# Optimization experiments

Hardware: AMD Instinct MI355X
Metric: run time of the kernel (lower is better)

The kernel has to match this reference:

```python
import jax, jax.numpy as jnp
import numpy as np

N_WG = 512      # waveguides n
N_COL = 512     # mesh columns
M = N_WG // 2   # node slots per column (odd columns have one masked dummy)
N_NODE = N_COL * M
B = 8192        # batch of input fields
PI4 = np.pi / 4


def build_mesh_indices():
    """Rectangular (Clements-style) mesh: per-column (top, bottom, mask) arrays."""
    top = np.zeros((N_COL, M), np.int32)
    bottom = np.zeros((N_COL, M), np.int32)
    mask = np.zeros((N_COL, M), np.int32)
    for c in range(N_COL):
        if c % 2 == 0:
            t = np.arange(0, N_WG, 2, dtype=np.int32)
            top[c], bottom[c], mask[c] = t, t + 1, 1
        else:
            t = np.arange(1, N_WG - 1, 2, dtype=np.int32)
            k = len(t)
            top[c, :k], bottom[c, :k], mask[c, :k] = t, t + 1, 1
            # masked dummy slot uses otherwise-unused rows 0 and N_WG-1
            top[c, k:], bottom[c, k:] = 0, N_WG - 1
    return jnp.asarray(top), jnp.asarray(bottom), jnp.asarray(mask)


def setup_inputs() -> dict:
    key = jax.random.key(0)
    ks = jax.random.split(key, 6)
    top, bottom, mask = build_mesh_indices()
    return {
        "x": jax.random.normal(ks[0], (N_WG, B), dtype=jnp.float32),
        "thetas": 2 * np.pi * jax.random.uniform(ks[1], (N_NODE,), dtype=jnp.float32),
        "phis": 2 * np.pi * jax.random.uniform(ks[2], (N_NODE,), dtype=jnp.float32),
        "gammas": 2 * np.pi * jax.random.uniform(ks[3], (N_WG,), dtype=jnp.float32),
        "bs_errors": 0.01 * jax.random.normal(ks[4], (N_NODE, 2), dtype=jnp.float32),
        "loss_errors": -0.1 * jax.random.uniform(ks[5], (N_NODE, 2), dtype=jnp.float32),
        "top": top, "bottom": bottom, "mask": mask,
    }


def _dc_terms(bs_errors, loss_errors, side):
    """_parallel_dc: per-node directional-coupler 2x2 elements [N,4] complex."""
    ins = jnp.exp(jnp.log(10.0) * loss_errors[:, side] / 20.0)
    e = bs_errors[:, side]
    s, c = jnp.sin(PI4 + e), jnp.cos(PI4 + e)
    t11 = (ins * s).astype(jnp.complex64)
    t12 = ins * (1j * c)
    t21 = (1j * c).astype(jnp.complex64)
    t22 = s.astype(jnp.complex64)
    return jnp.stack([t11, t12, t21, t22], axis=-1)


def _transform(v, T, t, b, m):
    """_parallel_transform: masked 2x2 gather-multiply-scatter. T: [M,4] complex."""
    vt, vb = v[t], v[b]
    one_m = 1.0 - m
    s11 = (T[:, 0] * m + one_m)[:, None]
    s12 = (T[:, 1] * m)[:, None]
    s21 = (T[:, 2] * m)[:, None]
    s22 = (T[:, 3] * m + one_m)[:, None]
    return v.at[t].set(s11 * vt + s21 * vb).at[b].set(s12 * vt + s22 * vb)


def reference(x, thetas, phis, gammas, bs_errors, loss_errors, top, bottom, mask):
    # input gamma phase screen, then propagate through all mesh columns
    v = x.astype(jnp.complex64) * jnp.exp(1j * gammas)[:, None]          # [n, B]
    left = _dc_terms(bs_errors, loss_errors, 0).reshape(N_COL, M, 4)
    right = _dc_terms(bs_errors, loss_errors, 1).reshape(N_COL, M, 4)
    th = thetas.reshape(N_COL, M)
    ph = phis.reshape(N_COL, M)
    mf = mask.astype(jnp.float32)

    def column(v, xs):
        t, b, m, thc, phc, L, R = xs
        # PhaseStyle.TOP, forward: phi -> left DC -> theta -> right DC
        v = v.at[t].multiply(jnp.exp(1j * phc * m)[:, None])
        v = _transform(v, L, t, b, m)
        v = v.at[t].multiply(jnp.exp(1j * thc * m)[:, None])
        v = _transform(v, R, t, b, m)
        return v, None

    v, _ = jax.lax.scan(column, v, (top, bottom, mf, th, ph, left, right))
    return jnp.stack([v.real, v.imag])  # [2, n, B]
```

## Files before the change

kernel.cpp:

```cpp
#include <hip/hip_runtime.h>
#include <math.h>

#define BATCH 8192
#define NROW 512
#define NCOL 512
#define MNODE 256

typedef __attribute__((ext_vector_type(8))) short bf16x8;
typedef __attribute__((ext_vector_type(4))) float f32x4;

__device__ __forceinline__ short2 split1(float x) {
  unsigned u = __float_as_uint(x);
  short h = (short)(u >> 16);
  float r = x - __uint_as_float(u & 0xffff0000u);
  short l = (short)(__float_as_uint(r) >> 16);
  return make_short2(h, l);
}

__global__ __launch_bounds__(256) void precomp_kernel(
    const float* __restrict__ thetas, const float* __restrict__ phis,
    const float* __restrict__ bse, const float* __restrict__ lse,
    float4* __restrict__ pp) {
  int n = blockIdx.x * 256 + threadIdx.x;
  float th = thetas[n], ph = phis[n];
  float e0 = bse[2 * n + 0], e1 = bse[2 * n + 1];
  float l0 = lse[2 * n + 0], l1 = lse[2 * n + 1];
  const float K = 0.16609640474436813f;
  float ins0 = exp2f(l0 * K), ins1 = exp2f(l1 * K);
  const float PI4 = 0.7853981633974483f;
  float s0, c0, s1, c1, sp, cp, st, ct;
  sincosf(PI4 + e0, &s0, &c0);
  sincosf(PI4 + e1, &s1, &c1);
  sincosf(ph, &sp, &cp);
  sincosf(th, &st, &ct);
  float AL = ins0 * s0, C1L = c0, C2L = ins0 * c0, SL = s0;
  float AR = ins1 * s1, C1R = c1, C2R = ins1 * c1, SR = s1;
  float a11r = AL * cp,   a11i = AL * sp;
  float a12r = 0.f,       a12i = C1L;
  float a21r = -C2L * sp, a21i = C2L * cp;
  float a22r = SL,        a22i = 0.f;
  float b11r = a11r * ct - a11i * st, b11i = a11r * st + a11i * ct;
  float b12r = a12r * ct - a12i * st, b12i = a12r * st + a12i * ct;
  float n11r = AR * b11r - C1R * a21i;
  float n11i = AR * b11i + C1R * a21r;
  float n12r = AR * b12r - C1R * a22i;
  float n12i = AR * b12i + C1R * a22r;
  float n21r = -C2R * b11i + SR * a21r;
  float n21i =  C2R * b11r + SR * a21i;
  float n22r = -C2R * b12i + SR * a22r;
  float n22i =  C2R * b12r + SR * a22i;
  pp[2 * n + 0] = make_float4(n11r, n11i, n12r, n12i);
  pp[2 * n + 1] = make_float4(n21r, n21i, n22r, n22i);
}

__device__ __forceinline__ void proc_pair(float& vtr, float& vti, float& vbr, float& vbi,
                                          const float4 q0, const float4 q1) {
  float tr = q0.x * vtr - q0.y * vti + q0.z * vbr - q0.w * vbi;
  float ti = q0.x * vti + q0.y * vtr + q0.z * vbi + q0.w * vbr;
  float br = q1.x * vtr - q1.y * vti + q1.z * vbr - q1.w * vbi;
  float bi = q1.x * vti + q1.y * vtr + q1.z * vbi + q1.w * vbr;
  vtr = tr; vti = ti; vbr = br; vbi = bi;
}

__device__ __forceinline__ int swz(int b) { return b ^ ((b >> 3) & 7); }

__global__ __launch_bounds__(256) void compose_band(
    const float* __restrict__ gammas, const float4* __restrict__ pp,
    float* __restrict__ Tsegs, int P) {
  __shared__ float ep[5120];

  const int tid  = threadIdx.x;
  const int lane = tid & 63;
  const int w    = tid >> 6;
  const int seg  = blockIdx.x >> 7;
  const int g    = blockIdx.x & 127;
  const int col  = g * 4 + w;

  const float4* ps = pp + (size_t)seg * P * 1024;
  float* T = Tsegs + (size_t)seg * (1024 * NROW);

  const int colA = (col - 63) & ~1;
  const int E    = colA + 2 * lane;
  const int je   = E >> 1;
  const int jeC  = je < 0 ? 0 : (je > 255 ? 255 : je);

  const bool vE  = (E >= 0) && (E <= 510);
  const bool vOT = (E >= 0) && (E <= 508);
  const bool vOB = (E >= 2) && (E <= 510);

  float ar = 0.f, ai = 0.f, br = 0.f, bi = 0.f;
  {
    float vr0 = 1.f, vi0 = 0.f;
    if (seg == 0) {
      float sg, cg;
      sincosf(gammas[col], &sg, &cg);
      vr0 = cg; vi0 = sg;
    }
    if (E == col)     { ar = vr0; ai = vi0; }
    if (E + 1 == col) { br = vr0; bi = vi0; }
  }

  const float4* pe = ps + 2 * jeC;
  const float4* po = ps + 512 + 2 * jeC;

  float sar = 0.f, sai = 0.f, sbr = 0.f, sbi = 0.f;

  for (int p = 0; p < P; ++p) {
    float4 q0 = pe[0];
    float4 q1 = pe[1];
    float4 o0 = po[0];
    float4 o1 = po[-1];
    pe += 1024; po += 1024;

    {
      float tr = q0.x * ar - q0.y * ai + q0.z * br - q0.w * bi;
      float ti = q0.x * ai + q0.y * ar + q0.z * bi + q0.w * br;
      float ur = q1.x * ar - q1.y * ai + q1.z * br - q1.w * bi;
      float ui = q1.x * ai + q1.y * ar + q1.z * bi + q1.w * br;
      if (vE) { ar = tr; ai = ti; br = ur; bi = ui; }
    }

    if (p == P - 1) { sar = ar; sai = ai; sbr = br; sbi = bi; }

    float anr = __shfl_down(ar, 1, 64);
    float ani = __shfl_down(ai, 1, 64);
    float bpr = __shfl_up(br, 1, 64);
    float bpi = __shfl_up(bi, 1, 64);
    if (lane == 63) { anr = 0.f; ani = 0.f; }
    if (lane == 0)  { bpr = 0.f; bpi = 0.f; }
    {
      float tr = o0.x * br - o0.y * bi + o0.z * anr - o0.w * ani;
      float ti = o0.x * bi + o0.y * br + o0.z * ani + o0.w * anr;
      float ur = o1.x * bpr - o1.y * bpi + o1.z * ar - o1.w * ai;
      float ui = o1.x * bpi + o1.y * bpr + o1.z * ai + o1.w * ar;
      if (vOT) { br = tr; bi = ti; }
      if (vOB) { ar = ur; ai = ui; }
    }
  }

  int sprow = -1;
  float spr = 0.f, spi = 0.f;
  if ((col & 1) == 0) {
    if (colA + 128 <= 511) {
      sprow = colA + 128;
      float4 w1 = ps[(size_t)(P - 1) * 1024 + 512 + 2 * (colA / 2 + 63) + 1];
      float vtr = __shfl(sbr, 63, 64);
      float vti = __shfl(sbi, 63, 64);
      spr = w1.x * vtr - w1.y * vti;
      spi = w1.x * vti + w1.y * vtr;
    }
  } else {
    if (colA - 1 >= 0) {
      sprow = colA - 1;
      float4 w0 = ps[(size_t)(P - 1) * 1024 + 512 + 2 * (colA / 2 - 1)];
      float vbr = __shfl(sar, 0, 64);
      float vbi = __shfl(sai, 0, 64);
      spr = w0.z * vbr - w0.w * vbi;
      spi = w0.z * vbi + w0.w * vbr;
    }
  }

  for (int i = tid; i < 5120; i += 256) ep[i] = 0.f;
  __syncthreads();
  if (E >= 0 && E <= 510) {
    ep[E * 5 + w]         = ar;
    ep[(512 + E) * 5 + w] = ai;
    ep[(E + 1) * 5 + w]       = br;
    ep[(513 + E) * 5 + w]     = bi;
  }
  if (lane == 0 && sprow >= 0) {
    ep[sprow * 5 + w]         = spr;
    ep[(512 + sprow) * 5 + w] = spi;
  }
  __syncthreads();
#pragma unroll
  for (int k = 0; k < 4; ++k) {
    const int i = k * 256 + tid;
    *(float4*)(T + (size_t)i * NROW + g * 4) =
        make_float4(ep[i * 5 + 0], ep[i * 5 + 1], ep[i * 5 + 2], ep[i * 5 + 3]);
  }
}

__global__ __launch_bounds__(256) void compose_kernel(
    const float* __restrict__ gammas, const float4* __restrict__ pp,
    float* __restrict__ Tsegs, int pairs_per_seg) {
  __shared__ float4 buf[2][1024];
  float* epf = (float*)buf;

  const int tid  = threadIdx.x;
  const int lane = tid & 63;
  const int w    = tid >> 6;
  const int seg  = blockIdx.x >> 7;
  const int g    = blockIdx.x & 127;
  const int col  = g * 4 + w;
  const int colmin = g * 4;

  const float4* ps = pp + (size_t)seg * pairs_per_seg * 1024;
  float* T = Tsegs + (size_t)seg * (1024 * NROW);

  float vr[8], vi[8];
#pragma unroll
  for (int r = 0; r < 8; ++r) {
    const int row = lane * 8 + r;
    vr[r] = 0.f; vi[r] = 0.f;
    if (row == col) {
      if (seg == 0) {
        float sg, cg;
        sincosf(gammas[row], &sg, &cg);
        vr[r] = cg; vi[r] = sg;
      } else {
        vr[r] = 1.f;
      }
    }
  }

  {
    const int sw = swz(tid);
#pragma unroll
    for (int k = 0; k < 4; ++k)
      buf[0][256 * k + sw] = ps[256 * k + tid];
  }
  __syncthreads();

  const int Lc = col >> 3;

#pragma unroll 1
  for (int p = 0; p < pairs_per_seg; ++p) {
    const int b = p & 1;

    const int HA = (p >> 2) + 3;
    const bool act  = (lane >= Lc - HA)     && (lane <= Lc + HA);
    const bool wide = (lane >= Lc - HA - 1) && (lane <= Lc + HA + 1);

    float4 f0, f1, f2, f3;
    bool st0 = false, st1 = false;
    if (p < pairs_per_seg - 1) {
      const int slo = colmin - 2 * p - 50;
      const int shi = colmin + 2 * p + 53;
      st0 = (tid + 1 >= slo) && (tid <= shi);
      st1 = (tid + 257 >= slo) && (tid + 256 <= shi);
      const float4* src = ps + (size_t)(p + 1) * 1024;
      if (st0) { f0 = src[tid];       f2 = src[512 + tid]; }
      if (st1) { f1 = src[256 + tid]; f3 = src[768 + tid]; }
    }

    float4 pe[8], po[7], pu1;
    if (act) {
      const int base = 8 * lane;
      const int l7 = lane & 7;
#pragma unroll
      for (int j = 0; j < 8; ++j) pe[j] = buf[b][base + (j ^ l7)];
#pragma unroll
      for (int j = 0; j < 7; ++j) po[j] = buf[b][512 + base + (j ^ l7)];
      const int lm = (lane == 0) ? 0 : lane - 1;
      pu1 = buf[b][512 + 8 * lm + (7 ^ (lm & 7))];

#pragma unroll
      for (int k = 0; k < 4; ++k)
        proc_pair(vr[2 * k], vi[2 * k], vr[2 * k + 1], vi[2 * k + 1],
                  pe[2 * k], pe[2 * k + 1]);

#pragma unroll
      for (int k = 0; k < 3; ++k)
        proc_pair(vr[2 * k + 1], vi[2 * k + 1], vr[2 * k + 2], vi[2 * k + 2],
                  po[2 * k], po[2 * k + 1]);
    }

    float br = 0.f, bi = 0.f, tu = 0.f, tv = 0.f;
    if (wide) {
      br = __shfl_down(vr[0], 1, 64);
      bi = __shfl_down(vi[0], 1, 64);
      tu = __shfl_up(vr[7], 1, 64);
      tv = __shfl_up(vi[7], 1, 64);
    }
    if (act) {
      float nAr = po[6].x * vr[7] - po[6].y * vi[7] + po[6].z * br - po[6].w * bi;
      float nAi = po[6].x * vi[7] + po[6].y * vr[7] + po[6].z * bi + po[6].w * br;
      float nBr = pu1.x * tu - pu1.y * tv + pu1.z * vr[0] - pu1.w * vi[0];
      float nBi = pu1.x * tv + pu1.y * tu + pu1.z * vi[0] + pu1.w * vr[0];
      if (lane < 63) { vr[7] = nAr; vi[7] = nAi; }
      if (lane > 0)  { vr[0] = nBr; vi[0] = nBi; }
    }

    if (p < pairs_per_seg - 1) {
      const int sw = swz(tid);
      if (st0) { buf[1 - b][sw] = f0;       buf[1 - b][512 + sw] = f2; }
      if (st1) { buf[1 - b][256 + sw] = f1; buf[1 - b][768 + sw] = f3; }
    }
    __syncthreads();
  }

#pragma unroll
  for (int r = 0; r < 8; ++r) {
    epf[(lane * 8 + r) * 5 + w] = vr[r];
    epf[(512 + lane * 8 + r) * 5 + w] = vi[r];
  }
  __syncthreads();
#pragma unroll
  for (int k = 0; k < 4; ++k) {
    const int i = k * 256 + tid;
    *(float4*)(T + (size_t)i * NROW + g * 4) =
        make_float4(epf[i * 5 + 0], epf[i * 5 + 1], epf[i * 5 + 2], epf[i * 5 + 3]);
  }
}

__global__ __launch_bounds__(256) void merge_g(
    const float* __restrict__ Ab, const float* __restrict__ Bb,
    float* __restrict__ Cb, long sA, long sB, long sC, int HA, int HB) {
  const float* A = Ab + (long)blockIdx.z * sA;
  const float* B = Bb + (long)blockIdx.z * sB;
  float*       C = Cb + (long)blockIdx.z * sC;

  __shared__ short sAh[64 * 40], sAl[64 * 40];

  const int tid = threadIdx.x;
  const int lane = tid & 63;
  const int w = tid >> 6;
  const int bm = blockIdx.y * 64;
  const int bn = blockIdx.x * 64;
  const int wm = (w & 1) * 32;
  const int wn = (w >> 1) * 32;
  const int q = lane >> 4;
  const int l15 = lane & 15;

  const int sm = tid >> 2;
  const int sk = (tid & 3) * 8;

  const int rmin = (blockIdx.y & 7) * 64;
  int klo = rmin - HA;
  {
    int t = bn - HB;
    if (t > klo) klo = t;
    if (klo < 0) klo = 0;
  }
  int khi = rmin + 63 + HA;
  {
    int t = bn + 63 + HB;
    if (t < khi) khi = t;
    if (khi > 511) khi = 511;
  }
  klo &= ~31;

  f32x4 acc[2][2];
#pragma unroll
  for (int i = 0; i < 2; ++i)
#pragma unroll
    for (int j = 0; j < 2; ++j) acc[i][j] = (f32x4){0.f, 0.f, 0.f, 0.f};

  if (klo <= khi) {
#pragma unroll 1
    for (int h = 0; h < 2; ++h) {
#pragma unroll 1
      for (int k0 = klo; k0 <= khi; k0 += 32) {
        const int gkb = h * 512 + k0;
        {
          const int gm = bm + sm;
          const int gk = gkb + sk;
          const int r = gm & 511;
          const bool top = gm < 512;
          const bool left = gk < 512;
          const int col = gk & 511;
          const float* src = (top == left) ? (A + (size_t)r * 512)
                                           : (A + (size_t)(512 + r) * 512);
          const float sgn = (top && !left) ? -1.f : 1.f;
          float4 v0 = *(const float4*)(src + col);
          float4 v1 = *(const float4*)(src + col + 4);
          float vv[8] = {v0.x, v0.y, v0.z, v0.w, v1.x, v1.y, v1.z, v1.w};
          short hh[8], ll[8];
#pragma unroll
          for (int i = 0; i < 8; ++i) {
            short2 s = split1(sgn * vv[i]);
            hh[i] = s.x; ll[i] = s.y;
          }
          __syncthreads();
          *(bf16x8*)&sAh[sm * 40 + sk] = *(bf16x8*)hh;
          *(bf16x8*)&sAl[sm * 40 + sk] = *(bf16x8*)ll;
          __syncthreads();
        }

        bf16x8 bh[2], bl[2];
#pragma unroll
        for (int nt = 0; nt < 2; ++nt) {
          const float* bp = B + (size_t)(gkb + q * 8) * 512 + bn + wn + nt * 16 + l15;
          short hh[8], ll[8];
#pragma unroll
          for (int j = 0; j < 8; ++j) {
            short2 s = split1(bp[(size_t)j * 512]);
            hh[j] = s.x; ll[j] = s.y;
          }
          bh[nt] = *(bf16x8*)hh;
          bl[nt] = *(bf16x8*)ll;
        }

        bf16x8 ah[2], al[2];
#pragma unroll
        for (int mt = 0; mt < 2; ++mt) {
          const int m = wm + mt * 16 + l15;
          ah[mt] = *(const bf16x8*)&sAh[m * 40 + q * 8];
          al[mt] = *(const bf16x8*)&sAl[m * 40 + q * 8];
        }

#pragma unroll
        for (int mt = 0; mt < 2; ++mt)
#pragma unroll
          for (int nt = 0; nt < 2; ++nt) {
            acc[mt][nt] = __builtin_amdgcn_mfma_f32_16x16x32_bf16(ah[mt], bh[nt], acc[mt][nt], 0, 0, 0);
            acc[mt][nt] = __builtin_amdgcn_mfma_f32_16x16x32_bf16(ah[mt], bl[nt], acc[mt][nt], 0, 0, 0);
            acc[mt][nt] = __builtin_amdgcn_mfma_f32_16x16x32_bf16(al[mt], bh[nt], acc[mt][nt], 0, 0, 0);
          }
      }
    }
  }

#pragma unroll
  for (int mt = 0; mt < 2; ++mt)
#pragma unroll
    for (int nt = 0; nt < 2; ++nt)
#pragma unroll
      for (int r = 0; r < 4; ++r) {
        const int gm = bm + wm + mt * 16 + q * 4 + r;
        const int gn = bn + wn + nt * 16 + l15;
        C[(size_t)gm * 512 + gn] = acc[mt][nt][r];
      }
}

__global__ __launch_bounds__(256) void xprep_kernel(
    const float* __restrict__ x, short* __restrict__ xp) {
  const int t = blockIdx.x * 256 + threadIdx.x;
  const int n = t & 8191;
  const int g = t >> 13;
  const float* src = x + (size_t)g * 8 * BATCH + n;
  short h[8], l[8];
#pragma unroll
  for (int j = 0; j < 8; ++j) {
    short2 s = split1(src[(size_t)j * BATCH]);
    h[j] = s.x; l[j] = s.y;
  }
  short* dst = xp + (size_t)t * 16;
  *(bf16x8*)dst = *(bf16x8*)h;
  *(bf16x8*)(dst + 8) = *(bf16x8*)l;
}

__global__ __launch_bounds__(256) void gemm_mfma_packed(
    const float* __restrict__ A, const short* __restrict__ xp,
    float* __restrict__ C) {
  __shared__ short sAh[64 * 40], sAl[64 * 40];

  const int tid = threadIdx.x;
  const int lane = tid & 63;
  const int w = tid >> 6;
  const int bm = blockIdx.y * 64;
  const int bn = blockIdx.x * 128;
  const int wm = (w & 1) * 32;
  const int wn = (w >> 1) * 64;
  const int q = lane >> 4;
  const int l15 = lane & 15;

  const int sm = tid >> 2;
  const int sk = (tid & 3) * 8;
  const float* Ap = A + (size_t)(bm + sm) * 512 + sk;

  f32x4 acc[2][4];
#pragma unroll
  for (int i = 0; i < 2; ++i)
#pragma unroll
    for (int j = 0; j < 4; ++j) acc[i][j] = (f32x4){0.f, 0.f, 0.f, 0.f};

  float4 pa[2];
  pa[0] = *(const float4*)(Ap);
  pa[1] = *(const float4*)(Ap + 4);

#pragma unroll 1
  for (int k0 = 0; k0 < 512; k0 += 32) {
    {
      short h[8], l[8];
#pragma unroll
      for (int i = 0; i < 8; ++i) {
        short2 s = split1(((const float*)pa)[i]);
        h[i] = s.x; l[i] = s.y;
      }
      __syncthreads();
      *(bf16x8*)&sAh[sm * 40 + sk] = *(bf16x8*)h;
      *(bf16x8*)&sAl[sm * 40 + sk] = *(bf16x8*)l;
      __syncthreads();
    }

    if (k0 + 32 < 512) {
      pa[0] = *(const float4*)(Ap + k0 + 32);
      pa[1] = *(const float4*)(Ap + k0 + 36);
    }

    const int kt = k0 >> 5;
    bf16x8 bh[4], bl[4];
#pragma unroll
    for (int nt = 0; nt < 4; ++nt) {
      const short* bp = xp + (((size_t)(kt * 4 + q)) * BATCH +
                              (bn + wn + nt * 16 + l15)) * 16;
      bh[nt] = *(const bf16x8*)bp;
      bl[nt] = *(const bf16x8*)(bp + 8);
    }

    bf16x8 ah[2], al[2];
#pragma unroll
    for (int mt = 0; mt < 2; ++mt) {
      const int m = wm + mt * 16 + l15;
      ah[mt] = *(const bf16x8*)&sAh[m * 40 + q * 8];
      al[mt] = *(const bf16x8*)&sAl[m * 40 + q * 8];
    }

#pragma unroll
    for (int mt = 0; mt < 2; ++mt)
#pragma unroll
      for (int nt = 0; nt < 4; ++nt) {
        acc[mt][nt] = __builtin_amdgcn_mfma_f32_16x16x32_bf16(ah[mt], bh[nt], acc[mt][nt], 0, 0, 0);
        acc[mt][nt] = __builtin_amdgcn_mfma_f32_16x16x32_bf16(ah[mt], bl[nt], acc[mt][nt], 0, 0, 0);
        acc[mt][nt] = __builtin_amdgcn_mfma_f32_16x16x32_bf16(al[mt], bh[nt], acc[mt][nt], 0, 0, 0);
      }
  }

#pragma unroll
  for (int mt = 0; mt < 2; ++mt)
#pragma unroll
    for (int nt = 0; nt < 4; ++nt)
#pragma unroll
      for (int r = 0; r < 4; ++r) {
        const int gm = bm + wm + mt * 16 + q * 4 + r;
        const int gn = bn + wn + nt * 16 + l15;
        C[(size_t)gm * BATCH + gn] = acc[mt][nt][r];
      }
}

__global__ __launch_bounds__(256) void gemm_mfma(
    const float* __restrict__ A, const float* __restrict__ B,
    float* __restrict__ C) {
  __shared__ short sAh[128 * 40], sAl[128 * 40];

  const int tid = threadIdx.x;
  const int lane = tid & 63;
  const int w = tid >> 6;
  const int bm = blockIdx.y * 128;
  const int bn = blockIdx.x * 128;
  const int wm = (w & 1) * 64;
  const int wn = (w >> 1) * 64;
  const int q = lane >> 4;
  const int l15 = lane & 15;

  const int sm = tid >> 1;
  const int sk = (tid & 1) * 16;
  const float* Ap = A + (size_t)(bm + sm) * 512 + sk;

  f32x4 acc[4][4];
#pragma unroll
  for (int i = 0; i < 4; ++i)
#pragma unroll
    for (int j = 0; j < 4; ++j) acc[i][j] = (f32x4){0.f, 0.f, 0.f, 0.f};

  float4 pa[4];
#pragma unroll
  for (int i = 0; i < 4; ++i) pa[i] = *(const float4*)(Ap + i * 4);

#pragma unroll 1
  for (int k0 = 0; k0 < 512; k0 += 32) {
    {
      short h[16], l[16];
#pragma unroll
      for (int i = 0; i < 16; ++i) {
        short2 s = split1(((const float*)pa)[i]);
        h[i] = s.x; l[i] = s.y;
      }
      __syncthreads();
      *(bf16x8*)&sAh[sm * 40 + sk]     = *(bf16x8*)&h[0];
      *(bf16x8*)&sAh[sm * 40 + sk + 8] = *(bf16x8*)&h[8];
      *(bf16x8*)&sAl[sm * 40 + sk]     = *(bf16x8*)&l[0];
      *(bf16x8*)&sAl[sm * 40 + sk + 8] = *(bf16x8*)&l[8];
      __syncthreads();
    }

    if (k0 + 32 < 512) {
#pragma unroll
      for (int i = 0; i < 4; ++i) pa[i] = *(const float4*)(Ap + k0 + 32 + i * 4);
    }

    bf16x8 bh[4], bl[4];
#pragma unroll
    for (int nt = 0; nt < 4; ++nt) {
      const float* bp = B + (size_t)(k0 + q * 8) * BATCH + bn + wn + nt * 16 + l15;
      short hh[8], ll[8];
#pragma unroll
      for (int j = 0; j < 8; ++j) {
        short2 s = split1(bp[(size_t)j * BATCH]);
        hh[j] = s.x; ll[j] = s.y;
      }
      bh[nt] = *(bf16x8*)hh;
      bl[nt] = *(bf16x8*)ll;
    }

    bf16x8 ah[4], al[4];
#pragma unroll
    for (int mt = 0; mt < 4; ++mt) {
      const int m = wm + mt * 16 + l15;
      ah[mt] = *(const bf16x8*)&sAh[m * 40 + q * 8];
      al[mt] = *(const bf16x8*)&sAl[m * 40 + q * 8];
    }

#pragma unroll
    for (int mt = 0; mt < 4; ++mt)
#pragma unroll
      for (int nt = 0; nt < 4; ++nt) {
        acc[mt][nt] = __builtin_amdgcn_mfma_f32_16x16x32_bf16(ah[mt], bh[nt], acc[mt][nt], 0, 0, 0);
        acc[mt][nt] = __builtin_amdgcn_mfma_f32_16x16x32_bf16(ah[mt], bl[nt], acc[mt][nt], 0, 0, 0);
        acc[mt][nt] = __builtin_amdgcn_mfma_f32_16x16x32_bf16(al[mt], bh[nt], acc[mt][nt], 0, 0, 0);
      }
  }

#pragma unroll
  for (int mt = 0; mt < 4; ++mt)
#pragma unroll
    for (int nt = 0; nt < 4; ++nt)
#pragma unroll
      for (int r = 0; r < 4; ++r) {
        const int gm = bm + wm + mt * 16 + q * 4 + r;
        const int gn = bn + wn + nt * 16 + l15;
        C[(size_t)gm * BATCH + gn] = acc[mt][nt][r];
      }
}

extern "C" void kernel_launch(void* const* d_in, const int* in_sizes, int n_in,
                              void* d_out, int out_size, void* d_ws, size_t ws_size,
                              hipStream_t stream) {
  const float* x      = (const float*)d_in[0];
  const float* thetas = (const float*)d_in[1];
  const float* phis   = (const float*)d_in[2];
  const float* gammas = (const float*)d_in[3];
  const float* bse    = (const float*)d_in[4];
  const float* lse    = (const float*)d_in[5];

  float* base = (float*)d_ws;
  float4* pp  = (float4*)d_ws;
  const long PPF   = 1048576;
  const long S     = 524288;

  precomp_kernel<<<512, 256, 0, stream>>>(thetas, phis, bse, lse, pp);

  if (ws_size >= (size_t)24 * 1024 * 1024) {
    float* segs = base + PPF;
    compose_band<<<1024, 256, 0, stream>>>(gammas, pp, segs, 32);

    float* U0 = base + 5 * PPF;
    float* U1 = base + 5 * PPF + S;
    float* U2 = base;
    float* U3 = base + S;
    merge_g<<<dim3(8, 16, 2), 256, 0, stream>>>(
        segs + S, segs, U0, 2 * S, 2 * S, S, 68, 68);
    merge_g<<<dim3(8, 16, 2), 256, 0, stream>>>(
        segs + 5 * S, segs + 4 * S, U2, 2 * S, 2 * S, S, 68, 68);
    float* V0 = base + PPF;
    float* V1 = base + PPF + S;
    merge_g<<<dim3(8, 16, 2), 256, 0, stream>>>(
        U1, U0, V0, (long)(U3 - U1), (long)(U2 - U0), S, 136, 136);
    float* Tf = base;
    merge_g<<<dim3(8, 16, 1), 256, 0, stream>>>(V1, V0, Tf, 0, 0, 0, 272, 272);

    short* xp = (short*)(base + S);
    xprep_kernel<<<2048, 256, 0, stream>>>(x, xp);

    gemm_mfma_packed<<<dim3(64, 16), 256, 0, stream>>>(Tf, xp, (float*)d_out);
  } else {
    int nseg;
    if (ws_size >= (size_t)14 * 1024 * 1024)      nseg = 4;
    else if (ws_size >= (size_t)8 * 1024 * 1024)  nseg = 2;
    else                                          nseg = 1;

    float* segs = base + PPF;
    float* Tf;
    compose_kernel<<<nseg * 128, 256, 0, stream>>>(gammas, pp, segs, 256 / nseg);

    if (nseg == 4) {
      float* T10 = base;
      float* T32 = base + S;
      Tf = segs + 4 * S;
      merge_g<<<dim3(8, 16, 2), 256, 0, stream>>>(
          segs + S, segs, T10, 2 * S, 2 * S, S, 132, 132);
      merge_g<<<dim3(8, 16, 1), 256, 0, stream>>>(
          T32, T10, Tf, 0, 0, 0, 264, 264);
    } else if (nseg == 2) {
      Tf = base;
      merge_g<<<dim3(8, 16, 1), 256, 0, stream>>>(
          segs + S, segs, Tf, 0, 0, 0, 260, 260);
    } else {
      Tf = segs;
    }

    gemm_mfma<<<dim3(BATCH / 128, 8), 256, 0, stream>>>(Tf, x, (float*)d_out);
  }
}
```

Measured before the change: 227.0 us.

## Store even segments pre-split in transposed bf16 layout and batch merges

The band-compose kernel now writes even segments as pre-split hi/lo bf16 arrays in a column-major layout, so the merge kernel loads its B operand directly as bf16x8 vectors instead of doing strided fp32 loads and splitting per element. A new merge_t kernel emits either fp32 (odd z) or pre-split bf16 (even z), which lets the four first-level merges run in one launch and cuts the merge tree from four launches to three. This removes redundant conversion work and strided global reads, at the cost of tricky workspace aliasing and buffer offsets.

Measured after the change: 231.2 us. About the same (+1.8%).

```diff
diff --git a/kernel.cpp b/kernel.cpp
--- a/kernel.cpp
+++ b/kernel.cpp
@@ -5,8 +5,10 @@
 #define NROW 512
 #define NCOL 512
 #define MNODE 256
+#define PL 524288
 
 typedef __attribute__((ext_vector_type(8))) short bf16x8;
+typedef __attribute__((ext_vector_type(4))) short s16x4;
 typedef __attribute__((ext_vector_type(4))) float f32x4;
 
 __device__ __forceinline__ short2 split1(float x) {
@@ -165,151 +167,53 @@
   if (E >= 0 && E <= 510) {
     ep[E * 5 + w]         = ar;
     ep[(512 + E) * 5 + w] = ai;
-    ep[(E + 1) * 5 + w]       = br;
-    ep[(513 + E) * 5 + w]     = bi;
+    ep[(E + 1) * 5 + w]   = br;
+    ep[(513 + E) * 5 + w] = bi;
   }
   if (lane == 0 && sprow >= 0) {
     ep[sprow * 5 + w]         = spr;
     ep[(512 + sprow) * 5 + w] = spi;
   }
   __syncthreads();
-#pragma unroll
-  for (int k = 0; k < 4; ++k) {
-    const int i = k * 256 + tid;
-    *(float4*)(T + (size_t)i * NROW + g * 4) =
-        make_float4(ep[i * 5 + 0], ep[i * 5 + 1], ep[i * 5 + 2], ep[i * 5 + 3]);
-  }
-}
-
-__global__ __launch_bounds__(256) void compose_kernel(
-    const float* __restrict__ gammas, const float4* __restrict__ pp,
-    float* __restrict__ Tsegs, int pairs_per_seg) {
-  __shared__ float4 buf[2][1024];
-  float* epf = (float*)buf;
-
-  const int tid  = threadIdx.x;
-  const int lane = tid & 63;
-  const int w    = tid >> 6;
-  const int seg  = blockIdx.x >> 7;
-  const int g    = blockIdx.x & 127;
-  const int col  = g * 4 + w;
-  const int colmin = g * 4;
-
-  const float4* ps = pp + (size_t)seg * pairs_per_seg * 1024;
-  float* T = Tsegs + (size_t)seg * (1024 * NROW);
-
-  float vr[8], vi[8];
-#pragma unroll
-  for (int r = 0; r < 8; ++r) {
-    const int row = lane * 8 + r;
-    vr[r] = 0.f; vi[r] = 0.f;
-    if (row == col) {
-      if (seg == 0) {
-        float sg, cg;
-        sincosf(gammas[row], &sg, &cg);
-        vr[r] = cg; vi[r] = sg;
-      } else {
-        vr[r] = 1.f;
-      }
-    }
-  }
-
-  {
-    const int sw = swz(tid);
-#pragma unroll
-    for (int k = 0; k < 4; ++k)
-      buf[0][256 * k + sw] = ps[256 * k + tid];
-  }
-  __syncthreads();
-
-  const int Lc = col >> 3;
-
-#pragma unroll 1
-  for (int p = 0; p < pairs_per_seg; ++p) {
-    const int b = p & 1;
-
-    const int HA = (p >> 2) + 3;
-    const bool act  = (lane >= Lc - HA)     && (lane <= Lc + HA);
-    const bool wide = (lane >= Lc - HA - 1) && (lane <= Lc + HA + 1);
-
-    float4 f0, f1, f2, f3;
-    bool st0 = false, st1 = false;
-    if (p < pairs_per_seg - 1) {
-      const int slo = colmin - 2 * p - 50;
-      const int shi = colmin + 2 * p + 53;
-      st0 = (tid + 1 >= slo) && (tid <= shi);
-      st1 = (tid + 257 >= slo) && (tid + 256 <= shi);
-      const float4* src = ps + (size_t)(p + 1) * 1024;
-      if (st0) { f0 = src[tid];       f2 = src[512 + tid]; }
-      if (st1) { f1 = src[256 + tid]; f3 = src[768 + tid]; }
-    }
-
-    float4 pe[8], po[7], pu1;
-    if (act) {
-      const int base = 8 * lane;
-      const int l7 = lane & 7;
-#pragma unroll
-      for (int j = 0; j < 8; ++j) pe[j] = buf[b][base + (j ^ l7)];
-#pragma unroll
-      for (int j = 0; j < 7; ++j) po[j] = buf[b][512 + base + (j ^ l7)];
-      const int lm = (lane == 0) ? 0 : lane - 1;
-      pu1 = buf[b][512 + 8 * lm + (7 ^ (lm & 7))];
-
-#pragma unroll
-      for (int k = 0; k < 4; ++k)
-        proc_pair(vr[2 * k], vi[2 * k], vr[2 * k + 1], vi[2 * k + 1],
-                  pe[2 * k], pe[2 * k + 1]);
-
-#pragma unroll
-      for (int k = 0; k < 3; ++k)
-        proc_pair(vr[2 * k + 1], vi[2 * k + 1], vr[2 * k + 2], vi[2 * k + 2],
-                  po[2 * k], po[2 * k + 1]);
-    }
-
-    float br = 0.f, bi = 0.f, tu = 0.f, tv = 0.f;
-    if (wide) {
-      br = __shfl_down(vr[0], 1, 64);
-      bi = __shfl_down(vi[0], 1, 64);
-      tu = __shfl_up(vr[7], 1, 64);
-      tv = __shfl_up(vi[7], 1, 64);
-    }
-    if (act) {
-      float nAr = po[6].x * vr[7] - po[6].y * vi[7] + po[6].z * br - po[6].w * bi;
-      float nAi = po[6].x * vi[7] + po[6].y * vr[7] + po[6].z * bi + po[6].w * br;
-      float nBr = pu1.x * tu - pu1.y * tv + pu1.z * vr[0] - pu1.w * vi[0];
-      float nBi = pu1.x * tv + pu1.y * tu + pu1.z * vi[0] + pu1.w * vr[0];
-      if (lane < 63) { vr[7] = nAr; vi[7] = nAi; }
-      if (lane > 0)  { vr[0] = nBr; vi[0] = nBi; }
-    }
-
-    if (p < pairs_per_seg - 1) {
-      const int sw = swz(tid);
-      if (st0) { buf[1 - b][sw] = f0;       buf[1 - b][512 + sw] = f2; }
-      if (st1) { buf[1 - b][256 + sw] = f1; buf[1 - b][768 + sw] = f3; }
-    }
-    __syncthreads();
-  }
-
-#pragma unroll
-  for (int r = 0; r < 8; ++r) {
-    epf[(lane * 8 + r) * 5 + w] = vr[r];
-    epf[(512 + lane * 8 + r) * 5 + w] = vi[r];
-  }
-  __syncthreads();
-#pragma unroll
-  for (int k = 0; k < 4; ++k) {
-    const int i = k * 256 + tid;
-    *(float4*)(T + (size_t)i * NROW + g * 4) =
-        make_float4(epf[i * 5 + 0], epf[i * 5 + 1], epf[i * 5 + 2], epf[i * 5 + 3]);
-  }
-}
-
-__global__ __launch_bounds__(256) void merge_g(
-    const float* __restrict__ Ab, const float* __restrict__ Bb,
-    float* __restrict__ Cb, long sA, long sB, long sC, int HA, int HB) {
-  const float* A = Ab + (long)blockIdx.z * sA;
-  const float* B = Bb + (long)blockIdx.z * sB;
-  float*       C = Cb + (long)blockIdx.z * sC;
+
+  if (seg & 1) {
+#pragma unroll
+    for (int k = 0; k < 4; ++k) {
+      const int i = k * 256 + tid;
+      *(float4*)(T + (size_t)i * NROW + g * 4) =
+          make_float4(ep[i * 5 + 0], ep[i * 5 + 1], ep[i * 5 + 2], ep[i * 5 + 3]);
+    }
+  } else {
+    unsigned short* Thi = (unsigned short*)T;
+    unsigned short* Tlo = Thi + PL;
+    const int c  = tid & 3;
+    const int k0 = (tid >> 2) * 16;
+    const int colg = g * 4 + c;
+    short hh[16], ll[16];
+#pragma unroll
+    for (int j = 0; j < 16; ++j) {
+      short2 s = split1(ep[(k0 + j) * 5 + c]);
+      hh[j] = s.x; ll[j] = s.y;
+    }
+    *(bf16x8*)&Thi[(size_t)colg * 1024 + k0]     = *(bf16x8*)&hh[0];
+    *(bf16x8*)&Thi[(size_t)colg * 1024 + k0 + 8] = *(bf16x8*)&hh[8];
+    *(bf16x8*)&Tlo[(size_t)colg * 1024 + k0]     = *(bf16x8*)&ll[0];
+    *(bf16x8*)&Tlo[(size_t)colg * 1024 + k0 + 8] = *(bf16x8*)&ll[8];
+  }
+}
+
+__global__ __launch_bounds__(256) void merge_t(
+    const float* __restrict__ Ab, long sA,
+    const unsigned short* __restrict__ Bb, long sB,
+    unsigned short* __restrict__ Cub, long sCu,
+    float* __restrict__ Cfb, long sCf,
+    int HA, int HB, int force_f) {
+  const int z = blockIdx.z;
+  const float* A = Ab + (long)z * sA;
+  const unsigned short* B = Bb + (long)z * sB;
+  const bool fout = force_f || (z & 1);
+  unsigned short* Cu = Cub + (long)(z >> 1) * sCu;
+  float*          Cf = Cfb + (long)(z >> 1) * sCf;
 
   __shared__ short sAh[64 * 40], sAl[64 * 40];
 
@@ -381,6 +285,264 @@
         bf16x8 bh[2], bl[2];
 #pragma unroll
         for (int nt = 0; nt < 2; ++nt) {
+          const unsigned short* bp =
+              B + (size_t)(bn + wn + nt * 16 + l15) * 1024 + gkb + q * 8;
+          bh[nt] = *(const bf16x8*)bp;
+          bl[nt] = *(const bf16x8*)(bp + PL);
+        }
+
+        bf16x8 ah[2], al[2];
+#pragma unroll
+        for (int mt = 0; mt < 2; ++mt) {
+          const int m = wm + mt * 16 + l15;
+          ah[mt] = *(const bf16x8*)&sAh[m * 40 + q * 8];
+          al[mt] = *(const bf16x8*)&sAl[m * 40 + q * 8];
+        }
+
+#pragma unroll
+        for (int mt = 0; mt < 2; ++mt)
+#pragma unroll
+          for (int nt = 0; nt < 2; ++nt) {
+            acc[mt][nt] = __builtin_amdgcn_mfma_f32_16x16x32_bf16(ah[mt], bh[nt], acc[mt][nt], 0, 0, 0);
+            acc[mt][nt] = __builtin_amdgcn_mfma_f32_16x16x32_bf16(ah[mt], bl[nt], acc[mt][nt], 0, 0, 0);
+            acc[mt][nt] = __builtin_amdgcn_mfma_f32_16x16x32_bf16(al[mt], bh[nt], acc[mt][nt], 0, 0, 0);
+          }
+      }
+    }
+  }
+
+  if (fout) {
+#pragma unroll
+    for (int mt = 0; mt < 2; ++mt)
+#pragma unroll
+      for (int nt = 0; nt < 2; ++nt)
+#pragma unroll
+        for (int r = 0; r < 4; ++r) {
+          const int gm = bm + wm + mt * 16 + q * 4 + r;
+          const int gn = bn + wn + nt * 16 + l15;
+          Cf[(size_t)gm * 512 + gn] = acc[mt][nt][r];
+        }
+  } else {
+    unsigned short* Chi = Cu;
+    unsigned short* Clo = Cu + PL;
+#pragma unroll
+    for (int mt = 0; mt < 2; ++mt)
+#pragma unroll
+      for (int nt = 0; nt < 2; ++nt) {
+        short hh[4], ll[4];
+#pragma unroll
+        for (int r = 0; r < 4; ++r) {
+          short2 s = split1(acc[mt][nt][r]);
+          hh[r] = s.x; ll[r] = s.y;
+        }
+        const int gm0 = bm + wm + mt * 16 + q * 4;
+        const int gn  = bn + wn + nt * 16 + l15;
+        *(s16x4*)&Chi[(size_t)gn * 1024 + gm0] = *(s16x4*)hh;
+        *(s16x4*)&Clo[(size_t)gn * 1024 + gm0] = *(s16x4*)ll;
+      }
+  }
+}
+
+__global__ __launch_bounds__(256) void compose_kernel(
+    const float* __restrict__ gammas, const float4* __restrict__ pp,
+    float* __restrict__ Tsegs, int pairs_per_seg) {
+  __shared__ float4 buf[2][1024];
+  float* epf = (float*)buf;
+
+  const int tid  = threadIdx.x;
+  const int lane = tid & 63;
+  const int w    = tid >> 6;
+  const int seg  = blockIdx.x >> 7;
+  const int g    = blockIdx.x & 127;
+  const int col  = g * 4 + w;
+  const int colmin = g * 4;
+
+  const float4* ps = pp + (size_t)seg * pairs_per_seg * 1024;
+  float* T = Tsegs + (size_t)seg * (1024 * NROW);
+
+  float vr[8], vi[8];
+#pragma unroll
+  for (int r = 0; r < 8; ++r) {
+    const int row = lane * 8 + r;
+    vr[r] = 0.f; vi[r] = 0.f;
+    if (row == col) {
+      if (seg == 0) {
+        float sg, cg;
+        sincosf(gammas[row], &sg, &cg);
+        vr[r] = cg; vi[r] = sg;
+      } else {
+        vr[r] = 1.f;
+      }
+    }
+  }
+
+  {
+    const int sw = swz(tid);
+#pragma unroll
+    for (int k = 0; k < 4; ++k)
+      buf[0][256 * k + sw] = ps[256 * k + tid];
+  }
+  __syncthreads();
+
+  const int Lc = col >> 3;
+
+#pragma unroll 1
+  for (int p = 0; p < pairs_per_seg; ++p) {
+    const int b = p & 1;
+
+    const int HA = (p >> 2) + 3;
+    const bool act  = (lane >= Lc - HA)     && (lane <= Lc + HA);
+    const bool wide = (lane >= Lc - HA - 1) && (lane <= Lc + HA + 1);
+
+    float4 f0, f1, f2, f3;
+    bool st0 = false, st1 = false;
+    if (p < pairs_per_seg - 1) {
+      const int slo = colmin - 2 * p - 50;
+      const int shi = colmin + 2 * p + 53;
+      st0 = (tid + 1 >= slo) && (tid <= shi);
+      st1 = (tid + 257 >= slo) && (tid + 256 <= shi);
+      const float4* src = ps + (size_t)(p + 1) * 1024;
+      if (st0) { f0 = src[tid];       f2 = src[512 + tid]; }
+      if (st1) { f1 = src[256 + tid]; f3 = src[768 + tid]; }
+    }
+
+    float4 pe[8], po[7], pu1;
+    if (act) {
+      const int base = 8 * lane;
+      const int l7 = lane & 7;
+#pragma unroll
+      for (int j = 0; j < 8; ++j) pe[j] = buf[b][base + (j ^ l7)];
+#pragma unroll
+      for (int j = 0; j < 7; ++j) po[j] = buf[b][512 + base + (j ^ l7)];
+      const int lm = (lane == 0) ? 0 : lane - 1;
+      pu1 = buf[b][512 + 8 * lm + (7 ^ (lm & 7))];
+
+#pragma unroll
+      for (int k = 0; k < 4; ++k)
+        proc_pair(vr[2 * k], vi[2 * k], vr[2 * k + 1], vi[2 * k + 1],
+                  pe[2 * k], pe[2 * k + 1]);
+
+#pragma unroll
+      for (int k = 0; k < 3; ++k)
+        proc_pair(vr[2 * k + 1], vi[2 * k + 1], vr[2 * k + 2], vi[2 * k + 2],
+                  po[2 * k], po[2 * k + 1]);
+    }
+
+    float br = 0.f, bi = 0.f, tu = 0.f, tv = 0.f;
+    if (wide) {
+      br = __shfl_down(vr[0], 1, 64);
+      bi = __shfl_down(vi[0], 1, 64);
+      tu = __shfl_up(vr[7], 1, 64);
+      tv = __shfl_up(vi[7], 1, 64);
+    }
+    if (act) {
+      float nAr = po[6].x * vr[7] - po[6].y * vi[7] + po[6].z * br - po[6].w * bi;
+      float nAi = po[6].x * vi[7] + po[6].y * vr[7] + po[6].z * bi + po[6].w * br;
+      float nBr = pu1.x * tu - pu1.y * tv + pu1.z * vr[0] - pu1.w * vi[0];
+      float nBi = pu1.x * tv + pu1.y * tu + pu1.z * vi[0] + pu1.w * vr[0];
+      if (lane < 63) { vr[7] = nAr; vi[7] = nAi; }
+      if (lane > 0)  { vr[0] = nBr; vi[0] = nBi; }
+    }
+
+    if (p < pairs_per_seg - 1) {
+      const int sw = swz(tid);
+      if (st0) { buf[1 - b][sw] = f0;       buf[1 - b][512 + sw] = f2; }
+      if (st1) { buf[1 - b][256 + sw] = f1; buf[1 - b][768 + sw] = f3; }
+    }
+    __syncthreads();
+  }
+
+#pragma unroll
+  for (int r = 0; r < 8; ++r) {
+    epf[(lane * 8 + r) * 5 + w] = vr[r];
+    epf[(512 + lane * 8 + r) * 5 + w] = vi[r];
+  }
+  __syncthreads();
+#pragma unroll
+  for (int k = 0; k < 4; ++k) {
+    const int i = k * 256 + tid;
+    *(float4*)(T + (size_t)i * NROW + g * 4) =
+        make_float4(epf[i * 5 + 0], epf[i * 5 + 1], epf[i * 5 + 2], epf[i * 5 + 3]);
+  }
+}
+
+__global__ __launch_bounds__(256) void merge_g(
+    const float* __restrict__ Ab, const float* __restrict__ Bb,
+    float* __restrict__ Cb, long sA, long sB, long sC, int HA, int HB) {
+  const float* A = Ab + (long)blockIdx.z * sA;
+  const float* B = Bb + (long)blockIdx.z * sB;
+  float*       C = Cb + (long)blockIdx.z * sC;
+
+  __shared__ short sAh[64 * 40], sAl[64 * 40];
+
+  const int tid = threadIdx.x;
+  const int lane = tid & 63;
+  const int w = tid >> 6;
+  const int bm = blockIdx.y * 64;
+  const int bn = blockIdx.x * 64;
+  const int wm = (w & 1) * 32;
+  const int wn = (w >> 1) * 32;
+  const int q = lane >> 4;
+  const int l15 = lane & 15;
+
+  const int sm = tid >> 2;
+  const int sk = (tid & 3) * 8;
+
+  const int rmin = (blockIdx.y & 7) * 64;
+  int klo = rmin - HA;
+  {
+    int t = bn - HB;
+    if (t > klo) klo = t;
+    if (klo < 0) klo = 0;
+  }
+  int khi = rmin + 63 + HA;
+  {
+    int t = bn + 63 + HB;
+    if (t < khi) khi = t;
+    if (khi > 511) khi = 511;
+  }
+  klo &= ~31;
+
+  f32x4 acc[2][2];
+#pragma unroll
+  for (int i = 0; i < 2; ++i)
+#pragma unroll
+    for (int j = 0; j < 2; ++j) acc[i][j] = (f32x4){0.f, 0.f, 0.f, 0.f};
+
+  if (klo <= khi) {
+#pragma unroll 1
+    for (int h = 0; h < 2; ++h) {
+#pragma unroll 1
+      for (int k0 = klo; k0 <= khi; k0 += 32) {
+        const int gkb = h * 512 + k0;
+        {
+          const int gm = bm + sm;
+          const int gk = gkb + sk;
+          const int r = gm & 511;
+          const bool top = gm < 512;
+          const bool left = gk < 512;
+          const int col = gk & 511;
+          const float* src = (top == left) ? (A + (size_t)r * 512)
+                                           : (A + (size_t)(512 + r) * 512);
+          const float sgn = (top && !left) ? -1.f : 1.f;
+          float4 v0 = *(const float4*)(src + col);
+          float4 v1 = *(const float4*)(src + col + 4);
+          float vv[8] = {v0.x, v0.y, v0.z, v0.w, v1.x, v1.y, v1.z, v1.w};
+          short hh[8], ll[8];
+#pragma unroll
+          for (int i = 0; i < 8; ++i) {
+            short2 s = split1(sgn * vv[i]);
+            hh[i] = s.x; ll[i] = s.y;
+          }
+          __syncthreads();
+          *(bf16x8*)&sAh[sm * 40 + sk] = *(bf16x8*)hh;
+          *(bf16x8*)&sAl[sm * 40 + sk] = *(bf16x8*)ll;
+          __syncthreads();
+        }
+
+        bf16x8 bh[2], bl[2];
+#pragma unroll
+        for (int nt = 0; nt < 2; ++nt) {
           const float* bp = B + (size_t)(gkb + q * 8) * 512 + bn + wn + nt * 16 + l15;
           short hh[8], ll[8];
 #pragma unroll
@@ -637,34 +799,31 @@
 
   float* base = (float*)d_ws;
   float4* pp  = (float4*)d_ws;
-  const long PPF   = 1048576;
-  const long S     = 524288;
+  const long PPF = 1048576;
+  const long S   = 524288;
 
   precomp_kernel<<<512, 256, 0, stream>>>(thetas, phis, bse, lse, pp);
 
   if (ws_size >= (size_t)24 * 1024 * 1024) {
-    float* segs = base + PPF;
-    compose_band<<<1024, 256, 0, stream>>>(gammas, pp, segs, 32);
-
-    float* U0 = base + 5 * PPF;
-    float* U1 = base + 5 * PPF + S;
-    float* U2 = base;
-    float* U3 = base + S;
-    merge_g<<<dim3(8, 16, 2), 256, 0, stream>>>(
-        segs + S, segs, U0, 2 * S, 2 * S, S, 68, 68);
-    merge_g<<<dim3(8, 16, 2), 256, 0, stream>>>(
-        segs + 5 * S, segs + 4 * S, U2, 2 * S, 2 * S, S, 68, 68);
-    float* V0 = base + PPF;
-    float* V1 = base + PPF + S;
-    merge_g<<<dim3(8, 16, 2), 256, 0, stream>>>(
-        U1, U0, V0, (long)(U3 - U1), (long)(U2 - U0), S, 136, 136);
-    float* Tf = base;
-    merge_g<<<dim3(8, 16, 1), 256, 0, stream>>>(V1, V0, Tf, 0, 0, 0, 272, 272);
+    float* B0 = base + PPF;
+    compose_band<<<1024, 256, 0, stream>>>(gammas, pp, B0, 32);
+
+    merge_t<<<dim3(8, 16, 4), 256, 0, stream>>>(
+        B0 + S, 2 * S, (const unsigned short*)B0, 4 * S,
+        (unsigned short*)base, 2 * S, base + 5 * PPF, S, 68, 68, 0);
+
+    merge_t<<<dim3(8, 16, 2), 256, 0, stream>>>(
+        base + 5 * PPF, S, (const unsigned short*)base, 2 * S,
+        (unsigned short*)(base + PPF), 0, base + PPF + S, 0, 136, 136, 0);
+
+    merge_t<<<dim3(8, 16, 1), 256, 0, stream>>>(
+        base + PPF + S, 0, (const unsigned short*)(base + PPF), 0,
+        (unsigned short*)base, 0, base, 0, 272, 272, 1);
 
     short* xp = (short*)(base + S);
     xprep_kernel<<<2048, 256, 0, stream>>>(x, xp);
 
-    gemm_mfma_packed<<<dim3(64, 16), 256, 0, stream>>>(Tf, xp, (float*)d_out);
+    gemm_mfma_packed<<<dim3(64, 16), 256, 0, stream>>>(base, xp, (float*)d_out);
   } else {
     int nseg;
     if (ws_size >= (size_t)14 * 1024 * 1024)      nseg = 4;
```
